# Kernel tuning notes

Hardware: AMD Instinct MI355X
Metric: run time of the kernel (lower is better)

Reference implementation:

```python
import jax, jax.numpy as jnp
import numpy as np

DIM = 768
CA = 192  # int(dim * mlp_ratio)
T = 8

def setup_inputs() -> dict:
    key = jax.random.key(0)
    ks = jax.random.split(key, 7)
    x = jax.random.normal(ks[0], (197, 128, DIM), dtype=jnp.float32)
    w1 = jax.random.normal(ks[1], (DIM, CA), dtype=jnp.float32) * 0.02
    b1 = jax.random.normal(ks[2], (CA,), dtype=jnp.float32) * 0.02
    conv_w = jax.random.normal(ks[3], (CA, 3), dtype=jnp.float32) * 0.02  # depthwise temporal kernel (3,1,1)
    conv_b = jax.random.normal(ks[4], (CA,), dtype=jnp.float32) * 0.02
    w2 = jax.random.normal(ks[5], (CA, DIM), dtype=jnp.float32) * 0.02
    b2 = jax.random.normal(ks[6], (DIM,), dtype=jnp.float32) * 0.02
    return {"x": x, "w1": w1, "b1": b1, "conv_w": conv_w, "conv_b": conv_b, "w2": w2, "b2": b2}

def reference(x, w1, b1, conv_w, conv_b, w2, b2):
    # x: (L, BT, dim), tokens-first layout (fc1 applied before permute)
    x_id = x
    h = x @ w1 + b1                      # (L, BT, Ca)
    h = jnp.transpose(h, (1, 0, 2))      # (BT, L, Ca)
    BT, L, Ca = h.shape
    B = BT // T
    h = h[:, 1:, :]                      # drop first token (L-1 patch tokens)
    x_cls = h[:, :1, :]                  # (BT, 1, Ca) -- first token AFTER the slice (as in original)
    x_temp = h.reshape(B, T, L - 1, Ca)  # (B, T, P, Ca)
    # Depthwise Conv3d with kernel (3,1,1), pad (1,0,0): pure temporal depthwise conv.
    xp = jnp.pad(x_temp, ((0, 0), (1, 1), (0, 0), (0, 0)))
    x_after = (xp[:, :-2] * conv_w[:, 0] + xp[:, 1:-1] * conv_w[:, 1]
               + xp[:, 2:] * conv_w[:, 2] + conv_b)  # (B, T, P, Ca)
    # Triangular-masked pairwise diff: sum_{i<j} (x_after[j] - x_temp[i]) / 28,
    # computed without materializing the (B,T,T,P,Ca) diff tensor:
    # each x_after[j] appears j times; each x_temp[i] appears (T-1-i) times.
    t = jnp.arange(T, dtype=x.dtype)
    result = (jnp.einsum('t,btpc->bpc', t, x_after)
              - jnp.einsum('t,btpc->bpc', (T - 1) - t, x_temp)) / 28.0
    x_last = (x_temp + result[:, None]).reshape(BT, L - 1, Ca)
    out = jnp.concatenate([x_cls, x_last], axis=1)   # (BT, L, Ca)
    out = jnp.transpose(out, (1, 0, 2))              # (L, BT, Ca)
    out = jax.nn.gelu(out, approximate=False)        # torch nn.GELU default = exact erf
    out = out @ w2 + b2                              # (L, BT, dim)
    return x_id + out
```

## Files before the change

kernel.cpp:

```cpp
#include <hip/hip_runtime.h>
#include <hip/hip_bf16.h>
#include <math.h>

#define DIM   768
#define CA    192
#define NTOK  25216

typedef __attribute__((ext_vector_type(8))) short short8;
typedef __attribute__((ext_vector_type(4))) float f32x4;

static __device__ __forceinline__ short f2bf(float f) {
    union { __hip_bfloat16 b; short s; } u;
    u.b = __float2bfloat16(f);
    return u.s;
}
static __device__ __forceinline__ float gelu_exact(float x) {
    return 0.5f * x * (1.0f + erff(x * 0.70710678118654752440f));
}
static __device__ __forceinline__ void ld16(void* lds, const void* gsrc) {
    __builtin_amdgcn_global_load_lds((const __attribute__((address_space(1))) void*)gsrc,
                                     (__attribute__((address_space(3))) void*)lds, 16, 0, 0);
}

__global__ void prep_kernel(const float* __restrict__ w1, const float* __restrict__ w2,
                            short* __restrict__ w1T, short* __restrict__ w2T) {
    int idx = blockIdx.x * 256 + threadIdx.x;
    if (idx < CA * DIM) {
        int n = idx / DIM, k = idx - n * DIM;
        w1T[idx] = f2bf(w1[k * CA + n]);
        int n2 = idx / CA, k2 = idx - n2 * CA;
        w2T[idx] = f2bf(w2[k2 * DIM + n2]);
    }
}

__global__ __launch_bounds__(256, 2) void gemm1_fused(
        const float* __restrict__ x, const short* __restrict__ w1T,
        const float* __restrict__ b1, const float* __restrict__ conv_w,
        const float* __restrict__ conv_b, short* __restrict__ gq) {
    __shared__ __align__(16) short lds[3][10240];

    const int tid = threadIdx.x;
    const int bx  = blockIdx.x;
    const int l   = (bx >> 2) + 1;
    const int hm  = (bx >> 1) & 1;
    const int n0  = (bx & 1) * 96;
    const int R0  = l * 128 + hm * 64;

    const int wave = tid >> 6, lane = tid & 63;
    const int wm = wave >> 1, wn = wave & 1;
    const int lm = lane & 15, lg = lane >> 4;

    const short* bsrc[3];
    int bloff[3];
    #pragma unroll
    for (int j = 0; j < 3; j++) {
        int s3 = wave * 3 + j;
        int idx = s3 * 64 + lane;
        int m = idx >> 3, q = (idx & 7) ^ (m & 7);
        bsrc[j]  = w1T + (size_t)(n0 + m) * DIM + q * 8;
        bloff[j] = 4096 + s3 * 512;
    }

    const int ar  = tid >> 2;
    const int aq0 = (tid & 3) * 2;
    const float* xrow = x + (size_t)(R0 + ar) * DIM + aq0 * 8;

    f32x4 acc[2][3] = {};
    f32x4 a_regs[4];

    auto STAGE_B = [&](int t, int buf) {
        #pragma unroll
        for (int j = 0; j < 3; j++)
            ld16(&lds[buf][bloff[j]], bsrc[j] + t * 64);
    };
    auto WRITE_A = [&](int buf) {
        short8 lo, hi;
        #pragma unroll
        for (int e = 0; e < 4; e++) {
            lo[e] = f2bf(a_regs[0][e]); lo[4 + e] = f2bf(a_regs[1][e]);
            hi[e] = f2bf(a_regs[2][e]); hi[4 + e] = f2bf(a_regs[3][e]);
        }
        short* Ab = &lds[buf][0];
        *(short8*)&Ab[ar * 64 + ((aq0    ) ^ (ar & 7)) * 8] = lo;
        *(short8*)&Ab[ar * 64 + ((aq0 + 1) ^ (ar & 7)) * 8] = hi;
    };

    #pragma unroll
    for (int e = 0; e < 4; e++) a_regs[e] = *(const f32x4*)(xrow + e * 4);
    STAGE_B(0, 0);
    STAGE_B(1, 1);
    WRITE_A(0);
    #pragma unroll
    for (int e = 0; e < 4; e++) a_regs[e] = *(const f32x4*)(xrow + 64 + e * 4);

    #pragma unroll
    for (int t = 0; t < 12; t++) {
        if (t < 11) asm volatile("s_waitcnt vmcnt(7) lgkmcnt(0)" ::: "memory");
        else        asm volatile("s_waitcnt vmcnt(0) lgkmcnt(0)" ::: "memory");
        __builtin_amdgcn_s_barrier();
        if (t < 10) STAGE_B(t + 2, (t + 2) % 3);

        const short* A = &lds[t % 3][0];
        const short* B = &lds[t % 3][4096];
        short8 af[2][2], bf[3][2];
        #pragma unroll
        for (int i2 = 0; i2 < 2; i2++) {
            int r = wm * 32 + i2 * 16 + lm;
            #pragma unroll
            for (int ks = 0; ks < 2; ks++) {
                int c = ks * 4 + lg;
                af[i2][ks] = *(const short8*)&A[(r * 8 + (c ^ (r & 7))) * 8];
            }
        }
        #pragma unroll
        for (int j = 0; j < 3; j++) {
            int rB = wn * 48 + j * 16 + lm;
            #pragma unroll
            for (int ks = 0; ks < 2; ks++) {
                int c = ks * 4 + lg;
                bf[j][ks] = *(const short8*)&B[(rB * 8 + (c ^ (rB & 7))) * 8];
            }
        }
        #pragma unroll
        for (int ks = 0; ks < 2; ks++)
            #pragma unroll
            for (int i2 = 0; i2 < 2; i2++)
                #pragma unroll
                for (int j = 0; j < 3; j++)
                    acc[i2][j] = __builtin_amdgcn_mfma_f32_16x16x32_bf16(af[i2][ks], bf[j][ks], acc[i2][j], 0, 0, 0);

        if (t < 11) {
            WRITE_A((t + 1) % 3);
            if (t < 10) {
                const float* xn = xrow + (t + 2) * 64;
                #pragma unroll
                for (int e = 0; e < 4; e++) a_regs[e] = *(const f32x4*)(xn + e * 4);
            }
        }
    }

    const int g1 = lg & 1;
    #pragma unroll
    for (int j = 0; j < 3; j++) {
        const int c = n0 + wn * 48 + j * 16 + lm;
        const float b1c = b1[c];
        const float cw0 = conv_w[c * 3 + 0];
        const float cw1 = conv_w[c * 3 + 1];
        const float cw2 = conv_w[c * 3 + 2];
        const float cb  = conv_b[c];
        #pragma unroll
        for (int i2 = 0; i2 < 2; i2++) {
            float hv[4];
            #pragma unroll
            for (int r = 0; r < 4; r++) hv[r] = acc[i2][j][r] + b1c;
            float partial = 0.f;
            #pragma unroll
            for (int r = 0; r < 4; r++) {
                const int t = g1 * 4 + r;
                const float tf = (float)t;
                float coef = tf * cw1 - (7.0f - tf);
                if (t <= 6) coef += (tf + 1.0f) * cw0;
                if (t >= 1) coef += (tf - 1.0f) * cw2;
                partial += coef * hv[r];
            }
            const float full = partial + __shfl_xor(partial, 16);
            const float res = cb + full * (1.0f / 28.0f);
            const int row = R0 + wm * 32 + i2 * 16 + lg * 4;
            #pragma unroll
            for (int r = 0; r < 4; r++)
                gq[(size_t)(row + r) * CA + c] = f2bf(gelu_exact(hv[r] + res));
            if (l == 1) {
                const int bt = row - 128;
                #pragma unroll
                for (int r = 0; r < 4; r++)
                    gq[(size_t)(bt + r) * CA + c] = f2bf(gelu_exact(hv[r]));
            }
        }
    }
}

__global__ __launch_bounds__(256, 2) void gemm2_kernel(
        const short* __restrict__ gq, const short* __restrict__ w2T,
        const float* __restrict__ b2, const float* __restrict__ x,
        float* __restrict__ out) {
    __shared__ __align__(16) short lds[2][12288];

    const int tid = threadIdx.x;
    const int m0 = blockIdx.x * 64;
    const int n0 = blockIdx.y * 128;
    const int wave = tid >> 6, lane = tid & 63;
    const int wm = wave >> 1, wn = wave & 1;
    const int lm = lane & 15, lg = lane >> 4;

    const short* src[6];
    int loff[6];
    #pragma unroll
    for (int j = 0; j < 6; j++) {
        int s6 = wave * 6 + j;
        if (s6 < 8) {
            int idx = s6 * 64 + lane;
            int m = idx >> 3, q = (idx & 7) ^ (m & 7);
            src[j]  = gq + (size_t)(m0 + m) * CA + q * 8;
            loff[j] = s6 * 512;
        } else {
            int idx = (s6 - 8) * 64 + lane;
            int m = idx >> 3, q = (idx & 7) ^ (m & 7);
            src[j]  = w2T + (size_t)(n0 + m) * CA + q * 8;
            loff[j] = 4096 + (s6 - 8) * 512;
        }
    }

    f32x4 acc[2][4] = {};

    auto STAGE = [&](int t, int buf) {
        #pragma unroll
        for (int j = 0; j < 6; j++)
            ld16(&lds[buf][loff[j]], src[j] + t * 64);
    };

    STAGE(0, 0);

    #pragma unroll
    for (int t = 0; t < 3; t++) {
        asm volatile("s_waitcnt vmcnt(0)" ::: "memory");
        __builtin_amdgcn_s_barrier();
        if (t < 2) STAGE(t + 1, (t + 1) & 1);

        const short* A = &lds[t & 1][0];
        const short* B = &lds[t & 1][4096];
        #pragma unroll
        for (int kk = 0; kk < 2; kk++) {
            const int c = kk * 4 + lg;
            short8 af[2], bf[4];
            #pragma unroll
            for (int i2 = 0; i2 < 2; i2++) {
                int r = wm * 32 + i2 * 16 + lm;
                af[i2] = *(const short8*)&A[(r * 8 + (c ^ (r & 7))) * 8];
            }
            #pragma unroll
            for (int j = 0; j < 4; j++) {
                int rB = wn * 64 + j * 16 + lm;
                bf[j] = *(const short8*)&B[(rB * 8 + (c ^ (rB & 7))) * 8];
            }
            #pragma unroll
            for (int i2 = 0; i2 < 2; i2++)
                #pragma unroll
                for (int j = 0; j < 4; j++)
                    acc[i2][j] = __builtin_amdgcn_mfma_f32_16x16x32_bf16(af[i2], bf[j], acc[i2][j], 0, 0, 0);
        }
    }

    #pragma unroll
    for (int i2 = 0; i2 < 2; i2++) {
        const int row0 = m0 + wm * 32 + i2 * 16 + lg * 4;
        #pragma unroll
        for (int j = 0; j < 4; j++) {
            const int col = n0 + wn * 64 + j * 16 + lm;
            const float bias = b2[col];
            #pragma unroll
            for (int r = 0; r < 4; r++) {
                const size_t idx = (size_t)(row0 + r) * DIM + col;
                out[idx] = acc[i2][j][r] + x[idx] + bias;
            }
        }
    }
}

extern "C" void kernel_launch(void* const* d_in, const int* in_sizes, int n_in,
                              void* d_out, int out_size, void* d_ws, size_t ws_size,
                              hipStream_t stream) {
    (void)in_sizes; (void)n_in; (void)out_size; (void)ws_size;
    const float* x      = (const float*)d_in[0];
    const float* w1     = (const float*)d_in[1];
    const float* b1     = (const float*)d_in[2];
    const float* conv_w = (const float*)d_in[3];
    const float* conv_b = (const float*)d_in[4];
    const float* w2     = (const float*)d_in[5];
    const float* b2     = (const float*)d_in[6];
    float* out = (float*)d_out;

    char* ws = (char*)d_ws;
    short* g   = (short*)ws;
    short* w1T = (short*)(ws + 9682944);
    short* w2T = (short*)(ws + 9682944 + 294912);

    prep_kernel<<<(CA * DIM + 255) / 256, 256, 0, stream>>>(w1, w2, w1T, w2T);
    gemm1_fused<<<784, 256, 0, stream>>>(x, w1T, b1, conv_w, conv_b, g);
    gemm2_kernel<<<dim3(394, 6), 256, 0, stream>>>(g, w2T, b2, x, out);
}
```

Before: 197.1 us.

## Fuse fc1 and fc2 GEMMs into one kernel keeping GELU tile in LDS

```diff
diff --git a/kernel.cpp b/kernel.cpp
--- a/kernel.cpp
+++ b/kernel.cpp
@@ -4,7 +4,6 @@
 
 #define DIM   768
 #define CA    192
-#define NTOK  25216
 
 typedef __attribute__((ext_vector_type(8))) short short8;
 typedef __attribute__((ext_vector_type(4))) float f32x4;
@@ -33,116 +32,115 @@
     }
 }
 
-__global__ __launch_bounds__(256, 2) void gemm1_fused(
-        const float* __restrict__ x, const short* __restrict__ w1T,
-        const float* __restrict__ b1, const float* __restrict__ conv_w,
-        const float* __restrict__ conv_b, short* __restrict__ gq) {
-    __shared__ __align__(16) short lds[3][10240];
+__global__ __launch_bounds__(256, 2) void fused_kernel(
+        const float* __restrict__ x,    const short* __restrict__ w1T,
+        const float* __restrict__ b1,   const float* __restrict__ conv_w,
+        const float* __restrict__ conv_b, const short* __restrict__ w2T,
+        const float* __restrict__ b2,   short* __restrict__ g0s,
+        float* __restrict__ out) {
+    __shared__ __align__(16) short ldsbuf[36864];
+    short* pipe = ldsbuf;
+    short* gA   = ldsbuf + 24576;
 
     const int tid = threadIdx.x;
     const int bx  = blockIdx.x;
-    const int l   = (bx >> 2) + 1;
-    const int hm  = (bx >> 1) & 1;
-    const int n0  = (bx & 1) * 96;
+    const int l   = (bx >> 1) + 1;
+    const int hm  = bx & 1;
     const int R0  = l * 128 + hm * 64;
 
     const int wave = tid >> 6, lane = tid & 63;
     const int wm = wave >> 1, wn = wave & 1;
     const int lm = lane & 15, lg = lane >> 4;
 
-    const short* bsrc[3];
-    int bloff[3];
+    const short* b1src[3];
+    int b1lds[3];
     #pragma unroll
     for (int j = 0; j < 3; j++) {
-        int s3 = wave * 3 + j;
-        int idx = s3 * 64 + lane;
-        int m = idx >> 3, q = (idx & 7) ^ (m & 7);
-        bsrc[j]  = w1T + (size_t)(n0 + m) * DIM + q * 8;
-        bloff[j] = 4096 + s3 * 512;
-    }
-
-    const int ar  = tid >> 2;
-    const int aq0 = (tid & 3) * 2;
-    const float* xrow = x + (size_t)(R0 + ar) * DIM + aq0 * 8;
-
-    f32x4 acc[2][3] = {};
-    f32x4 a_regs[4];
-
-    auto STAGE_B = [&](int t, int buf) {
+        int s = (wave * 3 + j) * 64 + lane;
+        int m = s >> 2, q = (s & 3) ^ ((m >> 1) & 3);
+        b1src[j] = w1T + (size_t)m * DIM + q * 8;
+        b1lds[j] = 2048 + (wave * 3 + j) * 512;
+    }
+    const int ar    = tid >> 2;
+    const int q0    = tid & 3;
+    const int aslot = q0 ^ ((ar >> 1) & 3);
+    const float* xrow = x + (size_t)(R0 + ar) * DIM + q0 * 8;
+
+    f32x4 acc[2][6] = {};
+    f32x4 a_regs[3][2];
+
+    #pragma unroll
+    for (int st = 0; st < 3; st++) {
+        a_regs[st][0] = *(const f32x4*)(xrow + st * 32);
+        a_regs[st][1] = *(const f32x4*)(xrow + st * 32 + 4);
+    }
+    asm volatile("" ::: "memory");
+    #pragma unroll
+    for (int st = 0; st < 2; st++)
         #pragma unroll
         for (int j = 0; j < 3; j++)
-            ld16(&lds[buf][bloff[j]], bsrc[j] + t * 64);
-    };
-    auto WRITE_A = [&](int buf) {
-        short8 lo, hi;
-        #pragma unroll
-        for (int e = 0; e < 4; e++) {
-            lo[e] = f2bf(a_regs[0][e]); lo[4 + e] = f2bf(a_regs[1][e]);
-            hi[e] = f2bf(a_regs[2][e]); hi[4 + e] = f2bf(a_regs[3][e]);
-        }
-        short* Ab = &lds[buf][0];
-        *(short8*)&Ab[ar * 64 + ((aq0    ) ^ (ar & 7)) * 8] = lo;
-        *(short8*)&Ab[ar * 64 + ((aq0 + 1) ^ (ar & 7)) * 8] = hi;
-    };
-
-    #pragma unroll
-    for (int e = 0; e < 4; e++) a_regs[e] = *(const f32x4*)(xrow + e * 4);
-    STAGE_B(0, 0);
-    STAGE_B(1, 1);
-    WRITE_A(0);
-    #pragma unroll
-    for (int e = 0; e < 4; e++) a_regs[e] = *(const f32x4*)(xrow + 64 + e * 4);
-
-    #pragma unroll
-    for (int t = 0; t < 12; t++) {
-        if (t < 11) asm volatile("s_waitcnt vmcnt(7) lgkmcnt(0)" ::: "memory");
-        else        asm volatile("s_waitcnt vmcnt(0) lgkmcnt(0)" ::: "memory");
+            ld16(&pipe[st * 8192 + b1lds[j]], b1src[j] + st * 32);
+    asm volatile("" ::: "memory");
+    {
+        short8 v;
+        #pragma unroll
+        for (int e = 0; e < 4; e++) { v[e] = f2bf(a_regs[0][0][e]); v[4 + e] = f2bf(a_regs[0][1][e]); }
+        *(short8*)&pipe[0 * 8192 + ar * 32 + aslot * 8] = v;
+    }
+    a_regs[0][0] = *(const f32x4*)(xrow + 96);
+    a_regs[0][1] = *(const f32x4*)(xrow + 100);
+
+    #pragma unroll
+    for (int t = 0; t < 24; t++) {
+        if      (t == 0)  asm volatile("s_waitcnt vmcnt(5) lgkmcnt(0)" ::: "memory");
+        else if (t <= 20) asm volatile("s_waitcnt vmcnt(7) lgkmcnt(0)" ::: "memory");
+        else if (t == 21) asm volatile("s_waitcnt vmcnt(5) lgkmcnt(0)" ::: "memory");
+        else if (t == 22) asm volatile("s_waitcnt vmcnt(3) lgkmcnt(0)" ::: "memory");
+        else              asm volatile("s_waitcnt vmcnt(0) lgkmcnt(0)" ::: "memory");
         __builtin_amdgcn_s_barrier();
-        if (t < 10) STAGE_B(t + 2, (t + 2) % 3);
-
-        const short* A = &lds[t % 3][0];
-        const short* B = &lds[t % 3][4096];
-        short8 af[2][2], bf[3][2];
+
+        if (t <= 21) {
+            #pragma unroll
+            for (int j = 0; j < 3; j++)
+                ld16(&pipe[((t + 2) % 3) * 8192 + b1lds[j]], b1src[j] + (t + 2) * 32);
+        }
+        asm volatile("" ::: "memory");
+
+        const short* S = &pipe[(t % 3) * 8192];
+        short8 af[2], bf[6];
         #pragma unroll
         for (int i2 = 0; i2 < 2; i2++) {
             int r = wm * 32 + i2 * 16 + lm;
-            #pragma unroll
-            for (int ks = 0; ks < 2; ks++) {
-                int c = ks * 4 + lg;
-                af[i2][ks] = *(const short8*)&A[(r * 8 + (c ^ (r & 7))) * 8];
-            }
-        }
-        #pragma unroll
-        for (int j = 0; j < 3; j++) {
-            int rB = wn * 48 + j * 16 + lm;
-            #pragma unroll
-            for (int ks = 0; ks < 2; ks++) {
-                int c = ks * 4 + lg;
-                bf[j][ks] = *(const short8*)&B[(rB * 8 + (c ^ (rB & 7))) * 8];
-            }
-        }
-        #pragma unroll
-        for (int ks = 0; ks < 2; ks++)
-            #pragma unroll
-            for (int i2 = 0; i2 < 2; i2++)
-                #pragma unroll
-                for (int j = 0; j < 3; j++)
-                    acc[i2][j] = __builtin_amdgcn_mfma_f32_16x16x32_bf16(af[i2][ks], bf[j][ks], acc[i2][j], 0, 0, 0);
-
-        if (t < 11) {
-            WRITE_A((t + 1) % 3);
-            if (t < 10) {
-                const float* xn = xrow + (t + 2) * 64;
-                #pragma unroll
-                for (int e = 0; e < 4; e++) a_regs[e] = *(const f32x4*)(xn + e * 4);
+            af[i2] = *(const short8*)&S[r * 32 + (lg ^ ((r >> 1) & 3)) * 8];
+        }
+        #pragma unroll
+        for (int j = 0; j < 6; j++) {
+            int rB = wn * 96 + j * 16 + lm;
+            bf[j] = *(const short8*)&S[2048 + rB * 32 + (lg ^ ((rB >> 1) & 3)) * 8];
+        }
+        #pragma unroll
+        for (int i2 = 0; i2 < 2; i2++)
+            #pragma unroll
+            for (int j = 0; j < 6; j++)
+                acc[i2][j] = __builtin_amdgcn_mfma_f32_16x16x32_bf16(af[i2], bf[j], acc[i2][j], 0, 0, 0);
+
+        if (t <= 22) {
+            const int sl = (t + 1) % 3;
+            short8 v;
+            #pragma unroll
+            for (int e = 0; e < 4; e++) { v[e] = f2bf(a_regs[sl][0][e]); v[4 + e] = f2bf(a_regs[sl][1][e]); }
+            *(short8*)&pipe[sl * 8192 + ar * 32 + aslot * 8] = v;
+            if (t <= 19) {
+                a_regs[sl][0] = *(const f32x4*)(xrow + (t + 4) * 32);
+                a_regs[sl][1] = *(const f32x4*)(xrow + (t + 4) * 32 + 4);
             }
         }
     }
 
     const int g1 = lg & 1;
     #pragma unroll
-    for (int j = 0; j < 3; j++) {
-        const int c = n0 + wn * 48 + j * 16 + lm;
+    for (int j = 0; j < 6; j++) {
+        const int c = wn * 96 + j * 16 + lm;
         const float b1c = b1[c];
         const float cw0 = conv_w[c * 3 + 0];
         const float cw1 = conv_w[c * 3 + 1];
@@ -165,103 +163,99 @@
             }
             const float full = partial + __shfl_xor(partial, 16);
             const float res = cb + full * (1.0f / 28.0f);
-            const int row = R0 + wm * 32 + i2 * 16 + lg * 4;
-            #pragma unroll
-            for (int r = 0; r < 4; r++)
-                gq[(size_t)(row + r) * CA + c] = f2bf(gelu_exact(hv[r] + res));
+            const int mrow = wm * 32 + i2 * 16 + lg * 4;
+            #pragma unroll
+            for (int r = 0; r < 4; r++) {
+                const int m = mrow + r;
+                const int slot = (c >> 3) ^ (m & 7);
+                gA[m * 192 + slot * 8 + (c & 7)] = f2bf(gelu_exact(hv[r] + res));
+            }
             if (l == 1) {
-                const int bt = row - 128;
                 #pragma unroll
                 for (int r = 0; r < 4; r++)
-                    gq[(size_t)(bt + r) * CA + c] = f2bf(gelu_exact(hv[r]));
-            }
-        }
-    }
-}
-
-__global__ __launch_bounds__(256, 2) void gemm2_kernel(
-        const short* __restrict__ gq, const short* __restrict__ w2T,
-        const float* __restrict__ b2, const float* __restrict__ x,
-        float* __restrict__ out) {
-    __shared__ __align__(16) short lds[2][12288];
-
-    const int tid = threadIdx.x;
-    const int m0 = blockIdx.x * 64;
-    const int n0 = blockIdx.y * 128;
-    const int wave = tid >> 6, lane = tid & 63;
-    const int wm = wave >> 1, wn = wave & 1;
-    const int lm = lane & 15, lg = lane >> 4;
-
-    const short* src[6];
-    int loff[6];
+                    g0s[(size_t)(hm * 64 + mrow + r) * CA + c] = f2bf(gelu_exact(hv[r]));
+            }
+        }
+    }
+
+    int b2off[6], b2lds[6];
     #pragma unroll
     for (int j = 0; j < 6; j++) {
-        int s6 = wave * 6 + j;
-        if (s6 < 8) {
-            int idx = s6 * 64 + lane;
-            int m = idx >> 3, q = (idx & 7) ^ (m & 7);
-            src[j]  = gq + (size_t)(m0 + m) * CA + q * 8;
-            loff[j] = s6 * 512;
-        } else {
-            int idx = (s6 - 8) * 64 + lane;
-            int m = idx >> 3, q = (idx & 7) ^ (m & 7);
-            src[j]  = w2T + (size_t)(n0 + m) * CA + q * 8;
-            loff[j] = 4096 + (s6 - 8) * 512;
-        }
-    }
-
-    f32x4 acc[2][4] = {};
-
-    auto STAGE = [&](int t, int buf) {
+        int s = (wave * 6 + j) * 64 + lane;
+        int m = s / 24, q = s - m * 24;
+        b2off[j] = m * CA + (q ^ (m & 7)) * 8;
+        b2lds[j] = (wave * 6 + j) * 512;
+    }
+
+    const int npass = (l == 1) ? 2 : 1;
+    for (int pass = 0; pass < npass; pass++) {
+        const int RO = pass ? hm * 64 : R0;
+        if (pass == 1) {
+            asm volatile("s_waitcnt vmcnt(0) lgkmcnt(0)" ::: "memory");
+            __builtin_amdgcn_s_barrier();
+            #pragma unroll
+            for (int j = 0; j < 6; j++)
+                ld16(&gA[b2lds[j]], g0s + (size_t)hm * 64 * CA + b2off[j]);
+        }
         #pragma unroll
         for (int j = 0; j < 6; j++)
-            ld16(&lds[buf][loff[j]], src[j] + t * 64);
-    };
-
-    STAGE(0, 0);
-
-    #pragma unroll
-    for (int t = 0; t < 3; t++) {
-        asm volatile("s_waitcnt vmcnt(0)" ::: "memory");
-        __builtin_amdgcn_s_barrier();
-        if (t < 2) STAGE(t + 1, (t + 1) & 1);
-
-        const short* A = &lds[t & 1][0];
-        const short* B = &lds[t & 1][4096];
-        #pragma unroll
-        for (int kk = 0; kk < 2; kk++) {
-            const int c = kk * 4 + lg;
-            short8 af[2], bf[4];
-            #pragma unroll
-            for (int i2 = 0; i2 < 2; i2++) {
-                int r = wm * 32 + i2 * 16 + lm;
-                af[i2] = *(const short8*)&A[(r * 8 + (c ^ (r & 7))) * 8];
-            }
-            #pragma unroll
-            for (int j = 0; j < 4; j++) {
-                int rB = wn * 64 + j * 16 + lm;
-                bf[j] = *(const short8*)&B[(rB * 8 + (c ^ (rB & 7))) * 8];
-            }
+            ld16(&pipe[b2lds[j]], w2T + b2off[j]);
+
+        #pragma unroll
+        for (int nc = 0; nc < 12; nc++) {
+            asm volatile("s_waitcnt vmcnt(0) lgkmcnt(0)" ::: "memory");
+            __builtin_amdgcn_s_barrier();
+            if (nc < 11) {
+                #pragma unroll
+                for (int j = 0; j < 6; j++)
+                    ld16(&pipe[((nc + 1) & 1) * 12288 + b2lds[j]],
+                         w2T + (size_t)(nc + 1) * 64 * CA + b2off[j]);
+            }
+            asm volatile("" ::: "memory");
+
+            float xv[2][2][4];
             #pragma unroll
             for (int i2 = 0; i2 < 2; i2++)
                 #pragma unroll
-                for (int j = 0; j < 4; j++)
-                    acc[i2][j] = __builtin_amdgcn_mfma_f32_16x16x32_bf16(af[i2], bf[j], acc[i2][j], 0, 0, 0);
-        }
-    }
-
-    #pragma unroll
-    for (int i2 = 0; i2 < 2; i2++) {
-        const int row0 = m0 + wm * 32 + i2 * 16 + lg * 4;
-        #pragma unroll
-        for (int j = 0; j < 4; j++) {
-            const int col = n0 + wn * 64 + j * 16 + lm;
-            const float bias = b2[col];
-            #pragma unroll
-            for (int r = 0; r < 4; r++) {
-                const size_t idx = (size_t)(row0 + r) * DIM + col;
-                out[idx] = acc[i2][j][r] + x[idx] + bias;
-            }
+                for (int j2 = 0; j2 < 2; j2++) {
+                    const int col = nc * 64 + wn * 32 + j2 * 16 + lm;
+                    #pragma unroll
+                    for (int r = 0; r < 4; r++)
+                        xv[i2][j2][r] = x[(size_t)(RO + wm * 32 + i2 * 16 + lg * 4 + r) * DIM + col];
+                }
+
+            const short* B2 = &pipe[(nc & 1) * 12288];
+            f32x4 acc2[2][2] = {};
+            #pragma unroll
+            for (int s2 = 0; s2 < 6; s2++) {
+                short8 af2[2], bf2[2];
+                #pragma unroll
+                for (int i2 = 0; i2 < 2; i2++) {
+                    int r = wm * 32 + i2 * 16 + lm;
+                    af2[i2] = *(const short8*)&gA[r * 192 + (((s2 * 4 + lg) ^ (r & 7))) * 8];
+                }
+                #pragma unroll
+                for (int j2 = 0; j2 < 2; j2++) {
+                    int rn = wn * 32 + j2 * 16 + lm;
+                    bf2[j2] = *(const short8*)&B2[rn * 192 + (((s2 * 4 + lg) ^ (rn & 7))) * 8];
+                }
+                #pragma unroll
+                for (int i2 = 0; i2 < 2; i2++)
+                    #pragma unroll
+                    for (int j2 = 0; j2 < 2; j2++)
+                        acc2[i2][j2] = __builtin_amdgcn_mfma_f32_16x16x32_bf16(af2[i2], bf2[j2], acc2[i2][j2], 0, 0, 0);
+            }
+            #pragma unroll
+            for (int i2 = 0; i2 < 2; i2++)
+                #pragma unroll
+                for (int j2 = 0; j2 < 2; j2++) {
+                    const int col = nc * 64 + wn * 32 + j2 * 16 + lm;
+                    const float bias = b2[col];
+                    #pragma unroll
+                    for (int r = 0; r < 4; r++)
+                        out[(size_t)(RO + wm * 32 + i2 * 16 + lg * 4 + r) * DIM + col] =
+                            acc2[i2][j2][r] + xv[i2][j2][r] + bias;
+                }
         }
     }
 }
@@ -280,11 +274,10 @@
     float* out = (float*)d_out;
 
     char* ws = (char*)d_ws;
-    short* g   = (short*)ws;
-    short* w1T = (short*)(ws + 9682944);
-    short* w2T = (short*)(ws + 9682944 + 294912);
+    short* w1T = (short*)ws;
+    short* w2T = (short*)(ws + 294912);
+    short* g0s = (short*)(ws + 589824);
 
     prep_kernel<<<(CA * DIM + 255) / 256, 256, 0, stream>>>(w1, w2, w1T, w2T);
-    gemm1_fused<<<784, 256, 0, stream>>>(x, w1T, b1, conv_w, conv_b, g);
-    gemm2_kernel<<<dim3(394, 6), 256, 0, stream>>>(g, w2T, b2, x, out);
-}
+    fused_kernel<<<392, 256, 0, stream>>>(x, w1T, b1, conv_w, conv_b, w2T, b2, g0s, out);
+}
```

Result: slower. 206.4 us (+4.7%).
